# Optimization experiments

Hardware: AMD Instinct MI355X
Metric: run time of the kernel (lower is better)

The kernel has to match this reference:

```python
import jax, jax.numpy as jnp
import numpy as np

B, T, E = 2, 2048, 1024
H, Dh = 16, 64  # num_heads, head_size; H*Dh == E


def setup_inputs() -> dict:
    key = jax.random.key(0)
    ks = jax.random.split(key, 5)
    s = 0.02
    return {
        "x": jax.random.normal(ks[0], (B, T, E), dtype=jnp.float32),
        "Wq": jax.random.normal(ks[1], (E, H * Dh), dtype=jnp.float32) * s,
        "Wk": jax.random.normal(ks[2], (E, H * Dh), dtype=jnp.float32) * s,
        "Wv": jax.random.normal(ks[3], (E, H * Dh), dtype=jnp.float32) * s,
        "Wo": jax.random.normal(ks[4], (H * Dh, E), dtype=jnp.float32) * s,
        "bo": jnp.zeros((E,), dtype=jnp.float32),
    }


def reference(x, Wq, Wk, Wv, Wo, bo):
    # Batched equivalent of the per-head Python loop: each head's bias-free
    # q/k/v Linear is one column-block of Wq/Wk/Wv.
    b, t, e = x.shape
    q = (x @ Wq).reshape(b, t, H, Dh)  # [B,T,H,Dh]
    k = (x @ Wk).reshape(b, t, H, Dh)
    v = (x @ Wv).reshape(b, t, H, Dh)

    scale = 1.0 / jnp.sqrt(jnp.asarray(Dh, dtype=x.dtype))
    scores = jnp.einsum("bqhd,bkhd->bhqk", q, k) * scale  # [B,H,T,T]
    causal = jnp.tril(jnp.ones((t, t), dtype=bool))
    scores = jnp.where(causal[None, None, :, :], scores, jnp.asarray(-jnp.inf, dtype=x.dtype))
    attn = jax.nn.softmax(scores, axis=-1)

    out = jnp.einsum("bhqk,bkhd->bqhd", attn, v).reshape(b, t, H * Dh)  # concat heads
    return out @ Wo + bo  # output projection (dropout is identity at p=0)
```

## Files before the change

### kernel.cpp

```cpp
#include <hip/hip_runtime.h>
#include <hip/hip_bf16.h>

typedef __attribute__((ext_vector_type(8))) short bf16x8;
typedef __attribute__((ext_vector_type(4))) float f32x4;
typedef __attribute__((ext_vector_type(4))) unsigned short u16x4;

__device__ __forceinline__ float bf2f(unsigned short u) {
    union { unsigned int i; float f; } x; x.i = ((unsigned int)u) << 16; return x.f;
}
__device__ __forceinline__ unsigned short f2bf(float f) {
    union { float f; unsigned int i; } x; x.f = f;
    unsigned int lsb = (x.i >> 16) & 1u;
    x.i += 0x7fffu + lsb;
    return (unsigned short)(x.i >> 16);
}

__device__ __forceinline__ void gl_lds16(const unsigned short* g, unsigned short* l) {
    __builtin_amdgcn_global_load_lds(
        (const __attribute__((address_space(1))) void*)g,
        (__attribute__((address_space(3))) void*)l, 16, 0, 0);
}

__global__ __launch_bounds__(256) void cvt_bf16(
    const float* __restrict__ in, unsigned short* __restrict__ out, int n4)
{
    int i = blockIdx.x * 256 + threadIdx.x;
    if (i < n4) {
        f32x4 v = ((const f32x4*)in)[i];
        u16x4 o;
#pragma unroll
        for (int j = 0; j < 4; ++j) o[j] = f2bf(v[j]);
        ((u16x4*)out)[i] = o;
    }
}

__global__ __launch_bounds__(256) void tconv(
    const float* __restrict__ in, unsigned short* __restrict__ out, int K, int N)
{
    __shared__ float t[32][33];
    const int tx = threadIdx.x & 31, ty = threadIdx.x >> 5;
    const int n0 = blockIdx.x * 32, k0 = blockIdx.y * 32;
#pragma unroll
    for (int i = 0; i < 4; ++i)
        t[ty + 8 * i][tx] = in[(size_t)(k0 + ty + 8 * i) * N + n0 + tx];
    __syncthreads();
#pragma unroll
    for (int i = 0; i < 4; ++i)
        out[(size_t)(n0 + ty + 8 * i) * K + k0 + tx] = f2bf(t[tx][ty + 8 * i]);
}

__global__ __launch_bounds__(256) void vtrans(
    const unsigned short* __restrict__ v, unsigned short* __restrict__ vT, int T)
{
    __shared__ __align__(16) unsigned short t[64][72];
    const int tid = threadIdx.x;
    const int bh = blockIdx.y;
    const int t0 = blockIdx.x * 64;
    const size_t base  = (size_t)bh * T * 64;
    const size_t tbase = (size_t)bh * 64 * T;
    const int r = tid >> 3, c = (tid & 7) * 8;
#pragma unroll
    for (int it = 0; it < 2; ++it)
        *(bf16x8*)&t[r + it * 32][c] =
            *(const bf16x8*)(v + base + (size_t)(t0 + r + it * 32) * 64 + c);
    __syncthreads();
#pragma unroll
    for (int it = 0; it < 2; ++it) {
        const int d = r + it * 32;
        bf16x8 o;
#pragma unroll
        for (int j = 0; j < 8; ++j) o[j] = t[c + j][d];
        *(bf16x8*)(vT + tbase + (size_t)d * T + t0 + c) = o;
    }
}

template <int PERM>
__global__ __launch_bounds__(256) void gemm128(
    const unsigned short* __restrict__ A,
    const unsigned short* __restrict__ BT,
    const float* __restrict__ bias,
    float* __restrict__ Cf,
    unsigned short* __restrict__ q_out,
    unsigned short* __restrict__ k_out,
    unsigned short* __restrict__ v_out,
    int M, int N, int K)
{
    __shared__ __align__(16) unsigned short As[128 * 32];
    __shared__ __align__(16) unsigned short Bs[128 * 32];

    const int tid  = threadIdx.x;
    const int wave = tid >> 6;
    const int lane = tid & 63;
    const int ln15 = lane & 15;
    const int kg   = lane >> 4;
    const int bm = blockIdx.x * 128, bn = blockIdx.y * 128;
    const int wm = (wave >> 1) * 64, wn = (wave & 1) * 64;

    f32x4 acc[4][4];
#pragma unroll
    for (int i = 0; i < 4; ++i)
#pragma unroll
        for (int j = 0; j < 4; ++j) acc[i][j] = (f32x4){0.f, 0.f, 0.f, 0.f};

    const int sr = wave * 32 + (lane >> 2);
    const int sc = (lane & 3) * 8;

    for (int k0 = 0; k0 < K; k0 += 32) {
        gl_lds16(A  + (size_t)(bm + sr)      * K + k0 + sc, As + wave * 1024);
        gl_lds16(A  + (size_t)(bm + sr + 16) * K + k0 + sc, As + wave * 1024 + 512);
        gl_lds16(BT + (size_t)(bn + sr)      * K + k0 + sc, Bs + wave * 1024);
        gl_lds16(BT + (size_t)(bn + sr + 16) * K + k0 + sc, Bs + wave * 1024 + 512);
        __syncthreads();

        bf16x8 af[4], bw[4];
#pragma unroll
        for (int mt = 0; mt < 4; ++mt)
            af[mt] = *(const bf16x8*)&As[(wm + mt * 16 + ln15) * 32 + kg * 8];
#pragma unroll
        for (int nt = 0; nt < 4; ++nt)
            bw[nt] = *(const bf16x8*)&Bs[(wn + nt * 16 + ln15) * 32 + kg * 8];
#pragma unroll
        for (int mt = 0; mt < 4; ++mt)
#pragma unroll
            for (int nt = 0; nt < 4; ++nt)
                acc[mt][nt] = __builtin_amdgcn_mfma_f32_16x16x32_bf16(
                    af[mt], bw[nt], acc[mt][nt], 0, 0, 0);
        __syncthreads();
    }

#pragma unroll
    for (int mt = 0; mt < 4; ++mt)
#pragma unroll
        for (int nt = 0; nt < 4; ++nt) {
            const int col = bn + wn + nt * 16 + ln15;
#pragma unroll
            for (int r = 0; r < 4; ++r) {
                const int row = bm + wm + mt * 16 + kg * 4 + r;
                float val = acc[mt][nt][r];
                if (PERM == 0) {
                    Cf[(size_t)row * N + col] = val + bias[col];
                } else {
                    const int sec = col >> 10;
                    const int h = (col >> 6) & 15, d = col & 63;
                    const int b = row >> 11, t = row & 2047;
                    const size_t idx = ((size_t)(b * 16 + h) * 2048 + t) * 64 + d;
                    if (sec == 0)      q_out[idx] = f2bf(val * 0.125f);
                    else if (sec == 1) k_out[idx] = f2bf(val);
                    else               v_out[idx] = f2bf(val);
                }
            }
        }
}

__device__ __forceinline__ unsigned int cvt_pk_bf16(float lo, float hi) {
    unsigned int d;
    asm("v_cvt_pk_bf16_f32 %0, %1, %2" : "=v"(d) : "v"(lo), "v"(hi));
    return d;
}

__device__ __forceinline__ bf16x8 pf_build(const f32x4& pa, const f32x4& pb) {
    unsigned int E0 = cvt_pk_bf16(pa[0], pa[1]);
    unsigned int O0 = cvt_pk_bf16(pa[2], pa[3]);
    unsigned int E1 = cvt_pk_bf16(pb[0], pb[1]);
    unsigned int O1 = cvt_pk_bf16(pb[2], pb[3]);
    asm("v_permlane32_swap_b32 %0, %1" : "+v"(E0), "+v"(E1));
    asm("v_permlane32_swap_b32 %0, %1" : "+v"(O0), "+v"(O1));
    asm("v_permlane16_swap_b32 %0, %1" : "+v"(E0), "+v"(E1));
    asm("v_permlane16_swap_b32 %0, %1" : "+v"(O0), "+v"(O1));
    union { unsigned int u[4]; bf16x8 v; } r;
    r.u[0] = E0; r.u[1] = O0; r.u[2] = E1; r.u[3] = O1;
    return r.v;
}

__device__ __forceinline__ void softmax_tile(
    f32x4 sr[4], bool diag, int q_loc, int kg,
    bf16x8& pf0, bf16x8& pf1, f32x4& accl, bf16x8 ones)
{
    if (diag) {
#pragma unroll
        for (int kt = 0; kt < 4; ++kt)
#pragma unroll
            for (int r = 0; r < 4; ++r)
                if (kt * 16 + kg * 4 + r > q_loc) sr[kt][r] = -1e30f;
    }
    f32x4 pe[4];
#pragma unroll
    for (int kt = 0; kt < 4; ++kt)
#pragma unroll
        for (int r = 0; r < 4; ++r) pe[kt][r] = __expf(sr[kt][r]);
    pf0 = pf_build(pe[0], pe[1]);
    pf1 = pf_build(pe[2], pe[3]);
    accl = __builtin_amdgcn_mfma_f32_16x16x32_bf16(pf0, ones, accl, 0, 0, 0);
    accl = __builtin_amdgcn_mfma_f32_16x16x32_bf16(pf1, ones, accl, 0, 0, 0);
}

__global__ __launch_bounds__(256) void flash_attn(
    const unsigned short* __restrict__ Q,
    const unsigned short* __restrict__ Km,
    const unsigned short* __restrict__ Vtg,
    unsigned short* __restrict__ O,
    int T, int H)
{
    __shared__ __align__(16) unsigned short Ks[2][64][72];
    __shared__ __align__(16) unsigned short Vs[2][64][72];

    const int tid  = threadIdx.x;
    const int wave = tid >> 6;
    const int lane = tid & 63;
    const int ln15 = lane & 15;
    const int kg   = lane >> 4;
    const int sA   = blockIdx.x;
    const int sB   = (T >> 6) - 1 - sA;
    const int kmax = sB;
    const int bh   = blockIdx.y;
    const int b    = bh >> 4, h = bh & 15;
    const size_t base  = (size_t)bh * T * 64;
    const size_t vbase = (size_t)bh * 64 * T;
    const int q_loc = wave * 16 + ln15;

    bf16x8 qf[2][2];
    {
        const unsigned short* QrA = Q + base + (size_t)(sA * 64 + q_loc) * 64;
        const unsigned short* QrB = Q + base + (size_t)(sB * 64 + q_loc) * 64;
        qf[0][0] = *(const bf16x8*)(QrA + kg * 8);
        qf[0][1] = *(const bf16x8*)(QrA + 32 + kg * 8);
        qf[1][0] = *(const bf16x8*)(QrB + kg * 8);
        qf[1][1] = *(const bf16x8*)(QrB + 32 + kg * 8);
    }

    bf16x8 ones;
    {
        const short o = (ln15 == 0) ? (short)0x3F80 : (short)0;
#pragma unroll
        for (int j = 0; j < 8; ++j) ones[j] = o;
    }

    f32x4 o_acc[2][4];
#pragma unroll
    for (int s = 0; s < 2; ++s)
#pragma unroll
        for (int dt = 0; dt < 4; ++dt) o_acc[s][dt] = (f32x4){0.f, 0.f, 0.f, 0.f};
    f32x4 acc_l[2] = {(f32x4){0.f, 0.f, 0.f, 0.f}, (f32x4){0.f, 0.f, 0.f, 0.f}};

    const int sky = tid >> 3;
    const int sd  = (tid & 7) * 8;

    bf16x8 pk0, pk1, pv0, pv1;
    pk0 = *(const bf16x8*)(Km + base + (size_t)sky * 64 + sd);
    pk1 = *(const bf16x8*)(Km + base + (size_t)(sky + 32) * 64 + sd);
    pv0 = *(const bf16x8*)(Vtg + vbase + (size_t)sky * T + sd);
    pv1 = *(const bf16x8*)(Vtg + vbase + (size_t)(sky + 32) * T + sd);

    for (int kb = 0; kb <= kmax; ++kb) {
        const int bufi = kb & 1;
        *(bf16x8*)&Ks[bufi][sky][sd]      = pk0;
        *(bf16x8*)&Ks[bufi][sky + 32][sd] = pk1;
        *(bf16x8*)&Vs[bufi][sky][sd]      = pv0;
        *(bf16x8*)&Vs[bufi][sky + 32][sd] = pv1;
        if (kb < kmax) {
            const int kn = (kb + 1) * 64;
            pk0 = *(const bf16x8*)(Km + base + (size_t)(kn + sky) * 64 + sd);
            pk1 = *(const bf16x8*)(Km + base + (size_t)(kn + sky + 32) * 64 + sd);
            pv0 = *(const bf16x8*)(Vtg + vbase + (size_t)sky * T + kn + sd);
            pv1 = *(const bf16x8*)(Vtg + vbase + (size_t)(sky + 32) * T + kn + sd);
        }
        __syncthreads();

        const bool doA = (kb <= sA);

        f32x4 srB[4], srA[4];
#pragma unroll
        for (int kt = 0; kt < 4; ++kt) {
            bf16x8 kf0 = *(const bf16x8*)&Ks[bufi][kt * 16 + ln15][kg * 8];
            bf16x8 kf1 = *(const bf16x8*)&Ks[bufi][kt * 16 + ln15][32 + kg * 8];
            f32x4 a = (f32x4){0.f, 0.f, 0.f, 0.f};
            a = __builtin_amdgcn_mfma_f32_16x16x32_bf16(kf0, qf[1][0], a, 0, 0, 0);
            a = __builtin_amdgcn_mfma_f32_16x16x32_bf16(kf1, qf[1][1], a, 0, 0, 0);
            srB[kt] = a;
            if (doA) {
                f32x4 c = (f32x4){0.f, 0.f, 0.f, 0.f};
                c = __builtin_amdgcn_mfma_f32_16x16x32_bf16(kf0, qf[0][0], c, 0, 0, 0);
                c = __builtin_amdgcn_mfma_f32_16x16x32_bf16(kf1, qf[0][1], c, 0, 0, 0);
                srA[kt] = c;
            }
        }

        bf16x8 pfB0, pfB1, pfA0, pfA1;
        softmax_tile(srB, kb == sB, q_loc, kg, pfB0, pfB1, acc_l[1], ones);
        if (doA)
            softmax_tile(srA, kb == sA, q_loc, kg, pfA0, pfA1, acc_l[0], ones);

#pragma unroll
        for (int dt = 0; dt < 4; ++dt) {
            bf16x8 vf0 = *(const bf16x8*)&Vs[bufi][dt * 16 + ln15][kg * 8];
            bf16x8 vf1 = *(const bf16x8*)&Vs[bufi][dt * 16 + ln15][32 + kg * 8];
            o_acc[1][dt] = __builtin_amdgcn_mfma_f32_16x16x32_bf16(pfB0, vf0, o_acc[1][dt], 0, 0, 0);
            o_acc[1][dt] = __builtin_amdgcn_mfma_f32_16x16x32_bf16(pfB1, vf1, o_acc[1][dt], 0, 0, 0);
            if (doA) {
                o_acc[0][dt] = __builtin_amdgcn_mfma_f32_16x16x32_bf16(pfA0, vf0, o_acc[0][dt], 0, 0, 0);
                o_acc[0][dt] = __builtin_amdgcn_mfma_f32_16x16x32_bf16(pfA1, vf1, o_acc[0][dt], 0, 0, 0);
            }
        }
    }

#pragma unroll
    for (int s = 0; s < 2; ++s) {
        const int qb = (s == 0 ? sA : sB) * 64;
        float inv[4];
#pragma unroll
        for (int r = 0; r < 4; ++r)
            inv[r] = 1.0f / __shfl(acc_l[s][r], lane & 48, 64);
#pragma unroll
        for (int dt = 0; dt < 4; ++dt)
#pragma unroll
            for (int r = 0; r < 4; ++r) {
                const int t = qb + wave * 16 + kg * 4 + r;
                const int d = dt * 16 + ln15;
                O[(size_t)(b * T + t) * (H * 64) + h * 64 + d] =
                    f2bf(o_acc[s][dt][r] * inv[r]);
            }
    }
}

extern "C" void kernel_launch(void* const* d_in, const int* in_sizes, int n_in,
                              void* d_out, int out_size, void* d_ws, size_t ws_size,
                              hipStream_t stream)
{
    const int B = 2, T = 2048, E = 1024, H = 16;
    const int M = B * T;

    const float* x  = (const float*)d_in[0];
    const float* Wq = (const float*)d_in[1];
    const float* Wk = (const float*)d_in[2];
    const float* Wv = (const float*)d_in[3];
    const float* Wo = (const float*)d_in[4];
    const float* bo = (const float*)d_in[5];
    float* out = (float*)d_out;

    unsigned short* xb     = (unsigned short*)d_ws;
    unsigned short* WqkvT  = xb + (size_t)M * E;
    unsigned short* WoT    = WqkvT + (size_t)3 * E * E;
    unsigned short* q      = WoT + (size_t)E * E;
    unsigned short* k      = q + (size_t)M * E;
    unsigned short* v      = k + (size_t)M * E;
    unsigned short* vT     = v + (size_t)M * E;
    unsigned short* ao     = vT + (size_t)M * E;

    cvt_bf16<<<(M * E / 4 + 255) / 256, 256, 0, stream>>>(x, xb, M * E / 4);
    dim3 tg(E / 32, E / 32);
    tconv<<<tg, 256, 0, stream>>>(Wq, WqkvT,                     E, E);
    tconv<<<tg, 256, 0, stream>>>(Wk, WqkvT + (size_t)E * E,     E, E);
    tconv<<<tg, 256, 0, stream>>>(Wv, WqkvT + (size_t)2 * E * E, E, E);
    tconv<<<tg, 256, 0, stream>>>(Wo, WoT,                       E, E);

    dim3 g1(M / 128, 3 * E / 128);
    gemm128<1><<<g1, 256, 0, stream>>>(xb, WqkvT, nullptr, nullptr, q, k, v,
                                       M, 3 * E, E);

    dim3 vg(T / 64, B * H);
    vtrans<<<vg, 256, 0, stream>>>(v, vT, T);

    dim3 ag(T / 128, B * H);
    flash_attn<<<ag, 256, 0, stream>>>(q, k, vT, ao, T, H);

    dim3 g2(M / 128, E / 128);
    gemm128<0><<<g2, 256, 0, stream>>>(ao, WoT, bo, out, nullptr, nullptr, nullptr,
                                       M, E, E);
}
```

Measured before the change: 197.1 us.

## Fuse prep kernels, write V transposed from QKV GEMM, vectorize epilogues

Merges the x conversion and the four weight transpose-convert launches into one prep kernel, which removes several launches. The QKV GEMM now writes V directly in transposed layout, so the separate vtrans kernel and the v buffer are gone. For the Q/K sections and the output projection it swaps MFMA operands so each lane holds contiguous columns, which lets the epilogue pack values with cvt_pk plus permlane swaps and issue vector stores instead of scattered scalar 2-byte or 4-byte stores. The extra branching and permutes slightly increase epilogue complexity.

New measurement: 208.7 us. 1.06x slower.

```diff
diff --git a/kernel.cpp b/kernel.cpp
--- a/kernel.cpp
+++ b/kernel.cpp
@@ -5,9 +5,6 @@
 typedef __attribute__((ext_vector_type(4))) float f32x4;
 typedef __attribute__((ext_vector_type(4))) unsigned short u16x4;
 
-__device__ __forceinline__ float bf2f(unsigned short u) {
-    union { unsigned int i; float f; } x; x.i = ((unsigned int)u) << 16; return x.f;
-}
 __device__ __forceinline__ unsigned short f2bf(float f) {
     union { float f; unsigned int i; } x; x.f = f;
     unsigned int lsb = (x.i >> 16) & 1u;
@@ -21,57 +18,61 @@
         (__attribute__((address_space(3))) void*)l, 16, 0, 0);
 }
 
-__global__ __launch_bounds__(256) void cvt_bf16(
-    const float* __restrict__ in, unsigned short* __restrict__ out, int n4)
-{
-    int i = blockIdx.x * 256 + threadIdx.x;
-    if (i < n4) {
-        f32x4 v = ((const f32x4*)in)[i];
+__device__ __forceinline__ unsigned int cvt_pk_bf16(float lo, float hi) {
+    unsigned int d;
+    asm("v_cvt_pk_bf16_f32 %0, %1, %2" : "=v"(d) : "v"(lo), "v"(hi));
+    return d;
+}
+
+__device__ __forceinline__ bf16x8 pf_build_s(f32x4 pa, f32x4 pb, float s) {
+    unsigned int E0 = cvt_pk_bf16(pa[0] * s, pa[1] * s);
+    unsigned int O0 = cvt_pk_bf16(pa[2] * s, pa[3] * s);
+    unsigned int E1 = cvt_pk_bf16(pb[0] * s, pb[1] * s);
+    unsigned int O1 = cvt_pk_bf16(pb[2] * s, pb[3] * s);
+    asm("v_permlane32_swap_b32 %0, %1" : "+v"(E0), "+v"(E1));
+    asm("v_permlane32_swap_b32 %0, %1" : "+v"(O0), "+v"(O1));
+    asm("v_permlane16_swap_b32 %0, %1" : "+v"(E0), "+v"(E1));
+    asm("v_permlane16_swap_b32 %0, %1" : "+v"(O0), "+v"(O1));
+    union { unsigned int u[4]; bf16x8 v; } r;
+    r.u[0] = E0; r.u[1] = O0; r.u[2] = E1; r.u[3] = O1;
+    return r.v;
+}
+
+__global__ __launch_bounds__(256) void prep(
+    const float* __restrict__ x,
+    const float* __restrict__ Wq, const float* __restrict__ Wk,
+    const float* __restrict__ Wv, const float* __restrict__ Wo,
+    unsigned short* __restrict__ xb,
+    unsigned short* __restrict__ WqkvT, unsigned short* __restrict__ WoT)
+{
+    const int E = 1024;
+    const int bid = blockIdx.x;
+    __shared__ float t[32][33];
+
+    if (bid < 4096) {
+        int i = bid * 256 + threadIdx.x;
+        f32x4 v = ((const f32x4*)x)[i];
         u16x4 o;
 #pragma unroll
         for (int j = 0; j < 4; ++j) o[j] = f2bf(v[j]);
-        ((u16x4*)out)[i] = o;
-    }
-}
-
-__global__ __launch_bounds__(256) void tconv(
-    const float* __restrict__ in, unsigned short* __restrict__ out, int K, int N)
-{
-    __shared__ float t[32][33];
+        ((u16x4*)xb)[i] = o;
+        return;
+    }
+    const int r = bid - 4096;
+    const int which = r >> 10;
+    const int sub = r & 1023;
+    const float* src = which == 0 ? Wq : which == 1 ? Wk : which == 2 ? Wv : Wo;
+    unsigned short* dst = which == 3 ? WoT : WqkvT + (size_t)which * E * E;
+
     const int tx = threadIdx.x & 31, ty = threadIdx.x >> 5;
-    const int n0 = blockIdx.x * 32, k0 = blockIdx.y * 32;
+    const int n0 = (sub & 31) * 32, k0 = (sub >> 5) * 32;
 #pragma unroll
     for (int i = 0; i < 4; ++i)
-        t[ty + 8 * i][tx] = in[(size_t)(k0 + ty + 8 * i) * N + n0 + tx];
+        t[ty + 8 * i][tx] = src[(size_t)(k0 + ty + 8 * i) * E + n0 + tx];
     __syncthreads();
 #pragma unroll
     for (int i = 0; i < 4; ++i)
-        out[(size_t)(n0 + ty + 8 * i) * K + k0 + tx] = f2bf(t[tx][ty + 8 * i]);
-}
-
-__global__ __launch_bounds__(256) void vtrans(
-    const unsigned short* __restrict__ v, unsigned short* __restrict__ vT, int T)
-{
-    __shared__ __align__(16) unsigned short t[64][72];
-    const int tid = threadIdx.x;
-    const int bh = blockIdx.y;
-    const int t0 = blockIdx.x * 64;
-    const size_t base  = (size_t)bh * T * 64;
-    const size_t tbase = (size_t)bh * 64 * T;
-    const int r = tid >> 3, c = (tid & 7) * 8;
-#pragma unroll
-    for (int it = 0; it < 2; ++it)
-        *(bf16x8*)&t[r + it * 32][c] =
-            *(const bf16x8*)(v + base + (size_t)(t0 + r + it * 32) * 64 + c);
-    __syncthreads();
-#pragma unroll
-    for (int it = 0; it < 2; ++it) {
-        const int d = r + it * 32;
-        bf16x8 o;
-#pragma unroll
-        for (int j = 0; j < 8; ++j) o[j] = t[c + j][d];
-        *(bf16x8*)(vT + tbase + (size_t)d * T + t0 + c) = o;
-    }
+        dst[(size_t)(n0 + ty + 8 * i) * E + k0 + tx] = f2bf(t[tx][ty + 8 * i]);
 }
 
 template <int PERM>
@@ -96,6 +97,8 @@
     const int bm = blockIdx.x * 128, bn = blockIdx.y * 128;
     const int wm = (wave >> 1) * 64, wn = (wave & 1) * 64;
 
+    const bool swap = (PERM == 0) || (bn < 2048);
+
     f32x4 acc[4][4];
 #pragma unroll
     for (int i = 0; i < 4; ++i)
@@ -119,57 +122,70 @@
 #pragma unroll
         for (int nt = 0; nt < 4; ++nt)
             bw[nt] = *(const bf16x8*)&Bs[(wn + nt * 16 + ln15) * 32 + kg * 8];
-#pragma unroll
-        for (int mt = 0; mt < 4; ++mt)
-#pragma unroll
-            for (int nt = 0; nt < 4; ++nt)
-                acc[mt][nt] = __builtin_amdgcn_mfma_f32_16x16x32_bf16(
-                    af[mt], bw[nt], acc[mt][nt], 0, 0, 0);
+        if (swap) {
+#pragma unroll
+            for (int mt = 0; mt < 4; ++mt)
+#pragma unroll
+                for (int nt = 0; nt < 4; ++nt)
+                    acc[mt][nt] = __builtin_amdgcn_mfma_f32_16x16x32_bf16(
+                        bw[nt], af[mt], acc[mt][nt], 0, 0, 0);
+        } else {
+#pragma unroll
+            for (int mt = 0; mt < 4; ++mt)
+#pragma unroll
+                for (int nt = 0; nt < 4; ++nt)
+                    acc[mt][nt] = __builtin_amdgcn_mfma_f32_16x16x32_bf16(
+                        af[mt], bw[nt], acc[mt][nt], 0, 0, 0);
+        }
         __syncthreads();
     }
 
-#pragma unroll
-    for (int mt = 0; mt < 4; ++mt)
-#pragma unroll
-        for (int nt = 0; nt < 4; ++nt) {
-            const int col = bn + wn + nt * 16 + ln15;
-#pragma unroll
-            for (int r = 0; r < 4; ++r) {
-                const int row = bm + wm + mt * 16 + kg * 4 + r;
-                float val = acc[mt][nt][r];
-                if (PERM == 0) {
-                    Cf[(size_t)row * N + col] = val + bias[col];
-                } else {
-                    const int sec = col >> 10;
-                    const int h = (col >> 6) & 15, d = col & 63;
-                    const int b = row >> 11, t = row & 2047;
-                    const size_t idx = ((size_t)(b * 16 + h) * 2048 + t) * 64 + d;
-                    if (sec == 0)      q_out[idx] = f2bf(val * 0.125f);
-                    else if (sec == 1) k_out[idx] = f2bf(val);
-                    else               v_out[idx] = f2bf(val);
+    if (PERM == 0) {
+#pragma unroll
+        for (int mt = 0; mt < 4; ++mt) {
+            const int row = bm + wm + mt * 16 + ln15;
+#pragma unroll
+            for (int nt = 0; nt < 4; ++nt) {
+                const int c0 = bn + wn + nt * 16 + kg * 4;
+                f32x4 bv = *(const f32x4*)(bias + c0);
+                f32x4 o;
+#pragma unroll
+                for (int r = 0; r < 4; ++r) o[r] = acc[mt][nt][r] + bv[r];
+                *(f32x4*)(Cf + (size_t)row * N + c0) = o;
+            }
+        }
+    } else {
+        const int sec = bn >> 10;
+        if (sec < 2) {
+            unsigned short* dst = sec == 0 ? q_out : k_out;
+            const float scale = sec == 0 ? 0.125f : 1.0f;
+#pragma unroll
+            for (int mt = 0; mt < 4; ++mt) {
+                const int tg = bm + wm + mt * 16 + ln15;
+                const int b = tg >> 11, t = tg & 2047;
+#pragma unroll
+                for (int np = 0; np < 2; ++np) {
+                    const int c0 = bn + wn + np * 32 + kg * 8;
+                    const int h = (c0 >> 6) & 15, d0 = c0 & 63;
+                    bf16x8 pf = pf_build_s(acc[mt][2 * np], acc[mt][2 * np + 1], scale);
+                    *(bf16x8*)(dst + ((size_t)(b * 16 + h) * 2048 + t) * 64 + d0) = pf;
                 }
             }
-        }
-}
-
-__device__ __forceinline__ unsigned int cvt_pk_bf16(float lo, float hi) {
-    unsigned int d;
-    asm("v_cvt_pk_bf16_f32 %0, %1, %2" : "=v"(d) : "v"(lo), "v"(hi));
-    return d;
-}
-
-__device__ __forceinline__ bf16x8 pf_build(const f32x4& pa, const f32x4& pb) {
-    unsigned int E0 = cvt_pk_bf16(pa[0], pa[1]);
-    unsigned int O0 = cvt_pk_bf16(pa[2], pa[3]);
-    unsigned int E1 = cvt_pk_bf16(pb[0], pb[1]);
-    unsigned int O1 = cvt_pk_bf16(pb[2], pb[3]);
-    asm("v_permlane32_swap_b32 %0, %1" : "+v"(E0), "+v"(E1));
-    asm("v_permlane32_swap_b32 %0, %1" : "+v"(O0), "+v"(O1));
-    asm("v_permlane16_swap_b32 %0, %1" : "+v"(E0), "+v"(E1));
-    asm("v_permlane16_swap_b32 %0, %1" : "+v"(O0), "+v"(O1));
-    union { unsigned int u[4]; bf16x8 v; } r;
-    r.u[0] = E0; r.u[1] = O0; r.u[2] = E1; r.u[3] = O1;
-    return r.v;
+        } else {
+#pragma unroll
+            for (int nt = 0; nt < 4; ++nt) {
+                const int c = bn + wn + nt * 16 + ln15;
+                const int h = (c >> 6) & 15, d = c & 63;
+#pragma unroll
+                for (int mp = 0; mp < 2; ++mp) {
+                    const int t0 = bm + wm + mp * 32 + kg * 8;
+                    const int b = t0 >> 11, t = t0 & 2047;
+                    bf16x8 pf = pf_build_s(acc[2 * mp][nt], acc[2 * mp + 1][nt], 1.0f);
+                    *(bf16x8*)(v_out + ((size_t)(b * 16 + h) * 64 + d) * 2048 + t) = pf;
+                }
+            }
+        }
+    }
 }
 
 __device__ __forceinline__ void softmax_tile(
@@ -188,8 +204,8 @@
     for (int kt = 0; kt < 4; ++kt)
 #pragma unroll
         for (int r = 0; r < 4; ++r) pe[kt][r] = __expf(sr[kt][r]);
-    pf0 = pf_build(pe[0], pe[1]);
-    pf1 = pf_build(pe[2], pe[3]);
+    pf0 = pf_build_s(pe[0], pe[1], 1.0f);
+    pf1 = pf_build_s(pe[2], pe[3], 1.0f);
     accl = __builtin_amdgcn_mfma_f32_16x16x32_bf16(pf0, ones, accl, 0, 0, 0);
     accl = __builtin_amdgcn_mfma_f32_16x16x32_bf16(pf1, ones, accl, 0, 0, 0);
 }
@@ -342,23 +358,14 @@
     unsigned short* WoT    = WqkvT + (size_t)3 * E * E;
     unsigned short* q      = WoT + (size_t)E * E;
     unsigned short* k      = q + (size_t)M * E;
-    unsigned short* v      = k + (size_t)M * E;
-    unsigned short* vT     = v + (size_t)M * E;
+    unsigned short* vT     = k + (size_t)M * E;
     unsigned short* ao     = vT + (size_t)M * E;
 
-    cvt_bf16<<<(M * E / 4 + 255) / 256, 256, 0, stream>>>(x, xb, M * E / 4);
-    dim3 tg(E / 32, E / 32);
-    tconv<<<tg, 256, 0, stream>>>(Wq, WqkvT,                     E, E);
-    tconv<<<tg, 256, 0, stream>>>(Wk, WqkvT + (size_t)E * E,     E, E);
-    tconv<<<tg, 256, 0, stream>>>(Wv, WqkvT + (size_t)2 * E * E, E, E);
-    tconv<<<tg, 256, 0, stream>>>(Wo, WoT,                       E, E);
+    prep<<<8192, 256, 0, stream>>>(x, Wq, Wk, Wv, Wo, xb, WqkvT, WoT);
 
     dim3 g1(M / 128, 3 * E / 128);
-    gemm128<1><<<g1, 256, 0, stream>>>(xb, WqkvT, nullptr, nullptr, q, k, v,
+    gemm128<1><<<g1, 256, 0, stream>>>(xb, WqkvT, nullptr, nullptr, q, k, vT,
                                        M, 3 * E, E);
-
-    dim3 vg(T / 64, B * H);
-    vtrans<<<vg, 256, 0, stream>>>(v, vT, T);
 
     dim3 ag(T / 128, B * H);
     flash_attn<<<ag, 256, 0, stream>>>(q, k, vT, ao, T, H);
```
